# Kernel optimization log

Hardware: AMD Instinct MI355X
Metric: run time of the kernel (lower is better)

Reference implementation:

```python
import jax, jax.numpy as jnp
import numpy as np

B, N, DIM, H = 1, 768, 384, 12
SK, SV, PK, PV, PD = 16, 16, 4, 4, 128
NUM_LOGITS = 3
SCALAR_SCALE = (NUM_LOGITS * SK) ** -0.5
POINT_SCALE = (NUM_LOGITS * PK * (9.0 / 2.0)) ** -0.5
PAIR_SCALE = NUM_LOGITS ** -0.5
EPS = 1e-8
SOFTPLUS_INV_1 = float(np.log(np.e - 1.0))  # torch init: log(exp(1)-1)


def setup_inputs() -> dict:
    key = jax.random.key(0)
    ks = jax.random.split(key, 16)
    w = lambda k, shape: (jax.random.normal(k, shape, jnp.float32) * 0.02)
    return {
        "single_repr": jax.random.normal(ks[0], (B, N, DIM), jnp.float32),
        "pairwise_repr": jax.random.normal(ks[1], (B, N, N, PD), jnp.float32),
        "rotations": jax.random.normal(ks[2], (B, N, 3, 3), jnp.float32),
        "translations": jax.random.normal(ks[3], (B, N, 3), jnp.float32),
        "mask": jnp.ones((B, N), dtype=bool),
        "Wq_s": w(ks[4], (DIM, H * SK)),
        "Wk_s": w(ks[5], (DIM, H * SK)),
        "Wv_s": w(ks[6], (DIM, H * SV)),
        "Wq_p": w(ks[7], (DIM, H * PK * 3)),
        "Wk_p": w(ks[8], (DIM, H * PK * 3)),
        "Wv_p": w(ks[9], (DIM, H * PV * 3)),
        "W_pair": w(ks[10], (PD, H)),
        "b_pair": jnp.zeros((H,), jnp.float32),
        "point_weights": jnp.full((H,), SOFTPLUS_INV_1, jnp.float32),
        "W_out": w(ks[11], (H * (SV + PD + PV * 4), DIM)),
        "b_out": jnp.zeros((DIM,), jnp.float32),
    }


def _ipa(single_repr, pairwise_repr, rotations, translations, mask,
         Wq_s, Wk_s, Wv_s, Wq_p, Wk_p, Wv_p, W_pair, b_pair,
         point_weights, W_out, b_out):
    x = single_repr
    # scalar q/k/v: (b,n,h*d) -> (b,h,n,d)
    heads_s = lambda t, d: t.reshape(B, N, H, d).transpose(0, 2, 1, 3)
    q_s = heads_s(x @ Wq_s, SK)
    k_s = heads_s(x @ Wk_s, SK)
    v_s = heads_s(x @ Wv_s, SV)
    # point q/k/v: (b,n,h*d*3) -> (b,h,n,d,3), then apply global frame
    heads_p = lambda t, d: t.reshape(B, N, H, d, 3).transpose(0, 2, 1, 3, 4)
    trans = translations[:, None, :, None, :]  # (b,1,n,1,3)
    to_global = lambda t: jnp.einsum('bhndc,bnrc->bhndr', t, rotations) + trans
    q_p = to_global(heads_p(x @ Wq_p, PK))
    k_p = to_global(heads_p(x @ Wk_p, PK))
    v_p = to_global(heads_p(x @ Wv_p, PV))

    logits = jnp.einsum('bhid,bhjd->bhij', q_s, k_s) * SCALAR_SCALE
    pair_bias = pairwise_repr @ W_pair + b_pair  # (b,i,j,h)
    logits = logits + pair_bias.transpose(0, 3, 1, 2) * PAIR_SCALE
    diff = q_p[:, :, :, None] - k_p[:, :, None]  # (b,h,i,j,d,3)
    point_dist = jnp.sum(diff * diff, axis=(-2, -1))  # (b,h,i,j)
    pw = jax.nn.softplus(point_weights)[None, :, None, None]
    logits = logits - 0.5 * POINT_SCALE * pw * point_dist

    m2 = (mask[:, :, None] & mask[:, None, :])[:, None]  # (b,1,i,j)
    logits = jnp.where(m2, logits, -jnp.finfo(logits.dtype).max)
    attn = jax.nn.softmax(logits, axis=-1)

    r_scalar = jnp.einsum('bhij,bhjd->bhid', attn, v_s)
    r_pair = jnp.einsum('bhij,bijd->bhid', attn, pairwise_repr)
    r_point = jnp.einsum('bhij,bhjdc->bhidc', attn, v_p) - trans
    # back to local frame: multiply by R^T
    r_point = jnp.einsum('bhndc,bncr->bhndr', r_point, rotations)
    r_pnorm = jnp.sqrt(jnp.sum(r_point * r_point, axis=-1) + EPS)

    flat = lambda t: t.transpose(0, 2, 1, 3).reshape(B, N, -1)
    f_point = r_point.transpose(0, 2, 1, 3, 4).reshape(B, N, -1)
    results = jnp.concatenate(
        [flat(r_scalar), f_point, flat(r_pnorm), flat(r_pair)], axis=-1)
    return results @ W_out + b_out


def reference(single_repr, pairwise_repr, rotations, translations, mask,
              Wq_s, Wk_s, Wv_s, Wq_p, Wk_p, Wv_p, W_pair, b_pair,
              point_weights, W_out, b_out):
    return _ipa(single_repr, pairwise_repr, rotations, translations, mask,
                Wq_s, Wk_s, Wv_s, Wq_p, Wk_p, Wv_p, W_pair, b_pair,
                point_weights, W_out, b_out)
```

## Files before the change

kernel.cpp:

```cpp
#include <hip/hip_runtime.h>
#include <math.h>

#define NRES 768
#define DIMM 384
#define NH   12

#define SCALAR_SCALE 0.14433756729740646f
#define HALF_POINT   0.06804138174397717f
#define PAIR_SCALE   0.5773502691896258f

__global__ __launch_bounds__(256) void k1_proj(
    const float* __restrict__ x, const float* __restrict__ rot, const float* __restrict__ trans,
    const float* __restrict__ Wqs, const float* __restrict__ Wks, const float* __restrict__ Wvs,
    const float* __restrict__ Wqp, const float* __restrict__ Wkp, const float* __restrict__ Wvp,
    float* __restrict__ qs, float* __restrict__ ks, float* __restrict__ vs,
    float* __restrict__ qpg, float* __restrict__ kpg, float* __restrict__ vpg)
{
    __shared__ float xs[4 * 384];
    __shared__ float xp[3][4][144];

    const int tid = threadIdx.x;
    const int n0 = blockIdx.x * 4;

    for (int idx = tid; idx < 384; idx += 256) {
        float4 v = ((const float4*)(x + (size_t)n0 * 384))[idx];
        ((float4*)xs)[idx] = v;
    }
    __syncthreads();

    if (tid < 252) {
        const int g = tid;
        int m, c0, wd;
        if (g < 144) { m = g / 48; c0 = (g - m * 48) * 4; wd = 192; }
        else { int z = g - 144; m = 3 + z / 36; c0 = (z - (m - 3) * 36) * 4; wd = 144; }
        const float* Wm = (m==0)?Wqs : (m==1)?Wks : (m==2)?Wvs : (m==3)?Wqp : (m==4)?Wkp : Wvp;
        const float* wp = Wm + c0;
        float acc[4][4] = {};
        #pragma unroll 2
        for (int k = 0; k < DIMM; ++k) {
            float4 w = *(const float4*)wp; wp += wd;
            #pragma unroll
            for (int r = 0; r < 4; ++r) {
                float xv = xs[r * 384 + k];
                acc[r][0] = fmaf(xv, w.x, acc[r][0]);
                acc[r][1] = fmaf(xv, w.y, acc[r][1]);
                acc[r][2] = fmaf(xv, w.z, acc[r][2]);
                acc[r][3] = fmaf(xv, w.w, acc[r][3]);
            }
        }
        if (m < 3) {
            float* dst = (m==0)?qs : (m==1)?ks : vs;
            #pragma unroll
            for (int r = 0; r < 4; ++r) {
                float4 st = make_float4(acc[r][0], acc[r][1], acc[r][2], acc[r][3]);
                *(float4*)(dst + (size_t)(n0 + r) * 192 + c0) = st;
            }
        } else {
            int mi = m - 3;
            #pragma unroll
            for (int r = 0; r < 4; ++r)
                #pragma unroll
                for (int u = 0; u < 4; ++u) xp[mi][r][c0 + u] = acc[r][u];
        }
    }
    __syncthreads();

    for (int t = tid; t < 576; t += 256) {
        int mi = t / 192; int rm = t - mi * 192; int r = rm / 48; int pt = rm - r * 48; int c0 = pt * 3;
        float p0 = xp[mi][r][c0+0], p1 = xp[mi][r][c0+1], p2 = xp[mi][r][c0+2];
        int n = n0 + r;
        const float* R = rot + n * 9; const float* T = trans + n * 3;
        float g0 = fmaf(R[0], p0, fmaf(R[1], p1, fmaf(R[2], p2, T[0])));
        float g1 = fmaf(R[3], p0, fmaf(R[4], p1, fmaf(R[5], p2, T[1])));
        float g2 = fmaf(R[6], p0, fmaf(R[7], p1, fmaf(R[8], p2, T[2])));
        float* dst = (mi==0)?qpg : (mi==1)?kpg : vpg;
        dst[n*144 + c0+0] = g0; dst[n*144 + c0+1] = g1; dst[n*144 + c0+2] = g2;
    }
}

__global__ __launch_bounds__(256, 3) void k2_attn(
    const float* __restrict__ pairwise, const float* __restrict__ rot, const float* __restrict__ trans,
    const float* __restrict__ Wp, const float* __restrict__ bp, const float* __restrict__ ptw,
    const float* __restrict__ qs, const float* __restrict__ ks, const float* __restrict__ vs,
    const float* __restrict__ qpg, const float* __restrict__ kpg, const float* __restrict__ vpg,
    float* __restrict__ results)
{
    __shared__ float Pt[64 * 129];
    __shared__ float PBp[4 * 64 * 13];
    __shared__ float E[64 * 13];
    __shared__ float Qs[192], Qp[144];
    __shared__ float mL[12], lL[12], aL[12], invL[12], hpL[12], bpL[12];
    __shared__ float rp_l[144];

    const int tid = threadIdx.x;
    const int i = blockIdx.x;
    const size_t ri = (size_t)i * 1920;

    if (tid < 48)                    ((float4*)Qs)[tid]      = ((const float4*)(qs  + (size_t)i * 192))[tid];
    if (tid >= 64 && tid < 100)      ((float4*)Qp)[tid - 64] = ((const float4*)(qpg + (size_t)i * 144))[tid - 64];
    if (tid >= 128 && tid < 140) {
        int h = tid - 128;
        hpL[h] = HALF_POINT * log1pf(__expf(ptw[h]));
        bpL[h] = PAIR_SCALE * bp[h];
        mL[h] = -3.0e38f; lL[h] = 0.f;
    }
    __syncthreads();

    const int j  = tid & 63;
    const int hg = tid >> 6;
    const int hh = tid >> 7, dpr = tid & 127, hb = hh * 6;

    float accp[6] = {0.f,0.f,0.f,0.f,0.f,0.f};
    float accs = 0.f, accq = 0.f;
    const int hs = tid >> 4;
    const int hq = tid / 12;

    for (int tile = 0; tile < 12; ++tile) {
        const int j0 = tile * 64;

        {
            const float4* Pg = (const float4*)(pairwise + ((size_t)i * NRES + j0) * 128);
            #pragma unroll
            for (int q = 0; q < 8; ++q) {
                int idx = tid + 256 * q;
                float4 v = Pg[idx];
                int row = idx >> 5, c4 = (idx & 31) << 2;
                float* dp = &Pt[row * 129 + c4];
                dp[0] = v.x; dp[1] = v.y; dp[2] = v.z; dp[3] = v.w;
            }
        }
        __syncthreads();

        {
            float pbp[12];
            #pragma unroll
            for (int h = 0; h < 12; ++h) pbp[h] = 0.f;
            const int d0 = hg * 32;
            #pragma unroll 4
            for (int d = 0; d < 32; ++d) {
                float p = Pt[j * 129 + d0 + d];
                const float* w = Wp + (d0 + d) * 12;
                #pragma unroll
                for (int h = 0; h < 12; ++h) pbp[h] = fmaf(p, w[h], pbp[h]);
            }
            const int jg = j0 + j;
            const float* kr = ks  + (size_t)jg * 192;
            const float* kp = kpg + (size_t)jg * 144;
            float own[3];
            #pragma unroll
            for (int e = 0; e < 3; ++e) {
                int h = 3 * hg + e;
                const float4* kv = (const float4*)(kr + h * 16);
                float4 a0 = kv[0], a1 = kv[1], a2 = kv[2], a3 = kv[3];
                const float4* qv = (const float4*)(Qs + h * 16);
                float4 q0 = qv[0], q1 = qv[1], q2 = qv[2], q3 = qv[3];
                float s = q0.x*a0.x + q0.y*a0.y + q0.z*a0.z + q0.w*a0.w
                        + q1.x*a1.x + q1.y*a1.y + q1.z*a1.z + q1.w*a1.w
                        + q2.x*a2.x + q2.y*a2.y + q2.z*a2.z + q2.w*a2.w
                        + q3.x*a3.x + q3.y*a3.y + q3.z*a3.z + q3.w*a3.w;
                const float4* pv = (const float4*)(kp + h * 12);
                float4 p0 = pv[0], p1 = pv[1], p2 = pv[2];
                const float4* qpv = (const float4*)(Qp + h * 12);
                float4 u0 = qpv[0], u1 = qpv[1], u2 = qpv[2];
                float d0v, dist;
                d0v = u0.x - p0.x; dist  = d0v*d0v;
                d0v = u0.y - p0.y; dist += d0v*d0v;
                d0v = u0.z - p0.z; dist += d0v*d0v;
                d0v = u0.w - p0.w; dist += d0v*d0v;
                d0v = u1.x - p1.x; dist += d0v*d0v;
                d0v = u1.y - p1.y; dist += d0v*d0v;
                d0v = u1.z - p1.z; dist += d0v*d0v;
                d0v = u1.w - p1.w; dist += d0v*d0v;
                d0v = u2.x - p2.x; dist += d0v*d0v;
                d0v = u2.y - p2.y; dist += d0v*d0v;
                d0v = u2.z - p2.z; dist += d0v*d0v;
                d0v = u2.w - p2.w; dist += d0v*d0v;
                own[e] = SCALAR_SCALE * s - hpL[h] * dist + bpL[h];
            }
            float* pbw = &PBp[hg * 832 + j * 13];
            #pragma unroll
            for (int h = 0; h < 12; ++h) {
                float v = PAIR_SCALE * pbp[h];
                if (h >= 3 * hg && h < 3 * hg + 3) v += own[h - 3 * hg];
                pbw[h] = v;
            }
        }
        __syncthreads();

        {
            const float* pbr = &PBp[j * 13];
            float Lv[3], tm[3];
            #pragma unroll
            for (int e = 0; e < 3; ++e) {
                int h = 3 * hg + e;
                Lv[e] = pbr[h] + pbr[832 + h] + pbr[1664 + h] + pbr[2496 + h];
                tm[e] = Lv[e];
            }
            #pragma unroll
            for (int o = 32; o > 0; o >>= 1) {
                #pragma unroll
                for (int e = 0; e < 3; ++e) tm[e] = fmaxf(tm[e], __shfl_xor(tm[e], o));
            }
            float ss[3], mnv[3], alv[3];
            #pragma unroll
            for (int e = 0; e < 3; ++e) {
                int h = 3 * hg + e;
                float mo = mL[h];
                float mn = fmaxf(mo, tm[e]);
                alv[e] = __expf(mo - mn);
                mnv[e] = mn;
                float ev = __expf(Lv[e] - mn);
                E[j * 13 + h] = ev;
                ss[e] = ev;
            }
            #pragma unroll
            for (int o = 32; o > 0; o >>= 1) {
                #pragma unroll
                for (int e = 0; e < 3; ++e) ss[e] += __shfl_xor(ss[e], o);
            }
            if (j == 0) {
                #pragma unroll
                for (int e = 0; e < 3; ++e) {
                    int h = 3 * hg + e;
                    mL[h] = mnv[e]; aL[h] = alv[e];
                    lL[h] = lL[h] * alv[e] + ss[e];
                }
            }
        }
        __syncthreads();

        {
            #pragma unroll
            for (int u = 0; u < 6; ++u) accp[u] *= aL[hb + u];
            #pragma unroll 4
            for (int jj = 0; jj < 64; ++jj) {
                float p = Pt[jj * 129 + dpr];
                const float* ej = &E[jj * 13 + hb];
                accp[0] = fmaf(ej[0], p, accp[0]);
                accp[1] = fmaf(ej[1], p, accp[1]);
                accp[2] = fmaf(ej[2], p, accp[2]);
                accp[3] = fmaf(ej[3], p, accp[3]);
                accp[4] = fmaf(ej[4], p, accp[4]);
                accp[5] = fmaf(ej[5], p, accp[5]);
            }
        }
        if (tid < 192) {
            accs *= aL[hs];
            const float* vb = vs + (size_t)j0 * 192 + tid;
            #pragma unroll 4
            for (int jj = 0; jj < 64; ++jj)
                accs = fmaf(E[jj * 13 + hs], vb[(size_t)jj * 192], accs);
        }
        if (tid < 144) {
            accq *= aL[hq];
            const float* vb = vpg + (size_t)j0 * 144 + tid;
            #pragma unroll 4
            for (int jj = 0; jj < 64; ++jj)
                accq = fmaf(E[jj * 13 + hq], vb[(size_t)jj * 144], accq);
        }
        __syncthreads();
    }

    if (tid < 12) invL[tid] = 1.0f / lL[tid];
    __syncthreads();

    #pragma unroll
    for (int u = 0; u < 6; ++u)
        results[ri + 384 + (size_t)(hb + u) * 128 + dpr] = accp[u] * invL[hb + u];

    if (tid < 192) results[ri + tid] = accs * invL[hs];

    if (tid < 144) {
        int pc = tid - hq * 12;
        int coord = pc - (pc / 3) * 3;
        rp_l[tid] = accq * invL[hq] - trans[i * 3 + coord];
    }
    __syncthreads();

    if (tid < 48) {
        int h = tid >> 2, d = tid & 3; int c0 = h * 12 + d * 3;
        float p0 = rp_l[c0], p1 = rp_l[c0 + 1], p2 = rp_l[c0 + 2];
        const float* R = rot + i * 9;
        float o0 = p0 * R[0] + p1 * R[3] + p2 * R[6];
        float o1 = p0 * R[1] + p1 * R[4] + p2 * R[7];
        float o2 = p0 * R[2] + p1 * R[5] + p2 * R[8];
        results[ri + 192 + c0 + 0] = o0;
        results[ri + 192 + c0 + 1] = o1;
        results[ri + 192 + c0 + 2] = o2;
        results[ri + 336 + h * 4 + d] = sqrtf(o0*o0 + o1*o1 + o2*o2 + 1e-8f);
    }
}

__global__ __launch_bounds__(384) void k3_out(
    const float* __restrict__ results, const float* __restrict__ Wo, const float* __restrict__ bo,
    float* __restrict__ out)
{
    __shared__ float As[4 * 1924];
    __shared__ float red[3 * 96 * 17];

    const int t = threadIdx.x;
    const int r0 = blockIdx.x * 4;

    #pragma unroll
    for (int q = 0; q < 5; ++q) {
        int idx = t + 384 * q;
        if (idx < 1920) {
            int r = idx / 480, c4 = idx - r * 480;
            float4 v = ((const float4*)(results + (size_t)(r0 + r) * 1920))[c4];
            float* dp = &As[r * 1924 + c4 * 4];
            dp[0] = v.x; dp[1] = v.y; dp[2] = v.z; dp[3] = v.w;
        }
    }
    __syncthreads();

    const int cg = t % 96, kp = t / 96;
    float acc[4][4] = {};
    const float* wp = Wo + (size_t)(kp * 480) * 384 + cg * 4;
    int ka = kp * 480;
    #pragma unroll 2
    for (int k = 0; k < 480; ++k, ++ka) {
        float4 w = *(const float4*)wp; wp += 384;
        #pragma unroll
        for (int r = 0; r < 4; ++r) {
            float a = As[r * 1924 + ka];
            acc[r][0] = fmaf(a, w.x, acc[r][0]);
            acc[r][1] = fmaf(a, w.y, acc[r][1]);
            acc[r][2] = fmaf(a, w.z, acc[r][2]);
            acc[r][3] = fmaf(a, w.w, acc[r][3]);
        }
    }
    if (kp > 0) {
        float* rp = &red[((kp - 1) * 96 + cg) * 17];
        #pragma unroll
        for (int r = 0; r < 4; ++r)
            #pragma unroll
            for (int u = 0; u < 4; ++u) rp[r * 4 + u] = acc[r][u];
    }
    __syncthreads();
    if (kp == 0) {
        float4 b = *(const float4*)(bo + cg * 4);
        #pragma unroll
        for (int r = 0; r < 4; ++r) {
            const float* r1 = &red[(0 * 96 + cg) * 17 + r * 4];
            const float* r2 = &red[(1 * 96 + cg) * 17 + r * 4];
            const float* r3 = &red[(2 * 96 + cg) * 17 + r * 4];
            float4 o;
            o.x = acc[r][0] + r1[0] + r2[0] + r3[0] + b.x;
            o.y = acc[r][1] + r1[1] + r2[1] + r3[1] + b.y;
            o.z = acc[r][2] + r1[2] + r2[2] + r3[2] + b.z;
            o.w = acc[r][3] + r1[3] + r2[3] + r3[3] + b.w;
            *(float4*)(out + (size_t)(r0 + r) * 384 + cg * 4) = o;
        }
    }
}

extern "C" void kernel_launch(void* const* d_in, const int* in_sizes, int n_in,
                              void* d_out, int out_size, void* d_ws, size_t ws_size,
                              hipStream_t stream) {
    const float* x        = (const float*)d_in[0];
    const float* pairwise = (const float*)d_in[1];
    const float* rot      = (const float*)d_in[2];
    const float* trans    = (const float*)d_in[3];
    const float* Wqs   = (const float*)d_in[5];
    const float* Wks   = (const float*)d_in[6];
    const float* Wvs   = (const float*)d_in[7];
    const float* Wqp   = (const float*)d_in[8];
    const float* Wkp   = (const float*)d_in[9];
    const float* Wvp   = (const float*)d_in[10];
    const float* Wp    = (const float*)d_in[11];
    const float* bp    = (const float*)d_in[12];
    const float* ptw   = (const float*)d_in[13];
    const float* Wo    = (const float*)d_in[14];
    const float* bo    = (const float*)d_in[15];
    float* out = (float*)d_out;

    float* ws = (float*)d_ws;
    float* qs      = ws;
    float* ksb     = qs   + 147456;
    float* vsb     = ksb  + 147456;
    float* qpg     = vsb  + 147456;
    float* kpg     = qpg  + 110592;
    float* vpg     = kpg  + 110592;
    float* results = vpg  + 110592;

    hipLaunchKernelGGL(k1_proj, dim3(192), dim3(256), 0, stream,
                       x, rot, trans, Wqs, Wks, Wvs, Wqp, Wkp, Wvp,
                       qs, ksb, vsb, qpg, kpg, vpg);
    hipLaunchKernelGGL(k2_attn, dim3(768), dim3(256), 0, stream,
                       pairwise, rot, trans, Wp, bp, ptw,
                       qs, ksb, vsb, qpg, kpg, vpg, results);
    hipLaunchKernelGGL(k3_out, dim3(192), dim3(384), 0, stream,
                       results, Wo, bo, out);
}
```

Baseline: 878.6 us.

## Split pair-bias into separate kernel and restructure attention, projection, and output GEMM

Adds a kernel that computes the pair bias for every (i,h,j) into a workspace buffer. The attention kernel then drops its LDS staging of the pairwise tile and its syncs, double-buffers the exp weights, and reads pairwise straight from global memory for the weighted sum. The projection kernel now handles 2 rows per block instead of 4, and the output GEMM handles 3 rows per block without the split-K reduction. The cost is reading the 300MB pairwise tensor twice (once for the bias, once for the aggregation), plus a fallback path used when the workspace is too small.

```diff
diff --git a/kernel.cpp b/kernel.cpp
--- a/kernel.cpp
+++ b/kernel.cpp
@@ -9,64 +9,53 @@
 #define HALF_POINT   0.06804138174397717f
 #define PAIR_SCALE   0.5773502691896258f
 
-__global__ __launch_bounds__(256) void k1_proj(
+__global__ __launch_bounds__(256) void k1_proj2(
     const float* __restrict__ x, const float* __restrict__ rot, const float* __restrict__ trans,
     const float* __restrict__ Wqs, const float* __restrict__ Wks, const float* __restrict__ Wvs,
     const float* __restrict__ Wqp, const float* __restrict__ Wkp, const float* __restrict__ Wvp,
     float* __restrict__ qs, float* __restrict__ ks, float* __restrict__ vs,
     float* __restrict__ qpg, float* __restrict__ kpg, float* __restrict__ vpg)
 {
-    __shared__ float xs[4 * 384];
-    __shared__ float xp[3][4][144];
+    __shared__ float xs[2 * 384];
+    __shared__ float xp[3][2][144];
 
     const int tid = threadIdx.x;
-    const int n0 = blockIdx.x * 4;
-
-    for (int idx = tid; idx < 384; idx += 256) {
-        float4 v = ((const float4*)(x + (size_t)n0 * 384))[idx];
-        ((float4*)xs)[idx] = v;
-    }
+    const int n0 = blockIdx.x * 2;
+
+    for (int idx = tid; idx < 192; idx += 256)
+        ((float4*)xs)[idx] = ((const float4*)(x + (size_t)n0 * 384))[idx];
     __syncthreads();
 
     if (tid < 252) {
-        const int g = tid;
         int m, c0, wd;
-        if (g < 144) { m = g / 48; c0 = (g - m * 48) * 4; wd = 192; }
-        else { int z = g - 144; m = 3 + z / 36; c0 = (z - (m - 3) * 36) * 4; wd = 144; }
+        if (tid < 144) { m = tid / 48; c0 = (tid - m * 48) * 4; wd = 192; }
+        else { int z = tid - 144; m = 3 + z / 36; c0 = (z - (m - 3) * 36) * 4; wd = 144; }
         const float* Wm = (m==0)?Wqs : (m==1)?Wks : (m==2)?Wvs : (m==3)?Wqp : (m==4)?Wkp : Wvp;
         const float* wp = Wm + c0;
-        float acc[4][4] = {};
-        #pragma unroll 2
+        float a00=0.f,a01=0.f,a02=0.f,a03=0.f, a10=0.f,a11=0.f,a12=0.f,a13=0.f;
+        #pragma unroll 4
         for (int k = 0; k < DIMM; ++k) {
             float4 w = *(const float4*)wp; wp += wd;
-            #pragma unroll
-            for (int r = 0; r < 4; ++r) {
-                float xv = xs[r * 384 + k];
-                acc[r][0] = fmaf(xv, w.x, acc[r][0]);
-                acc[r][1] = fmaf(xv, w.y, acc[r][1]);
-                acc[r][2] = fmaf(xv, w.z, acc[r][2]);
-                acc[r][3] = fmaf(xv, w.w, acc[r][3]);
-            }
+            float x0 = xs[k], x1 = xs[384 + k];
+            a00 = fmaf(x0, w.x, a00); a01 = fmaf(x0, w.y, a01);
+            a02 = fmaf(x0, w.z, a02); a03 = fmaf(x0, w.w, a03);
+            a10 = fmaf(x1, w.x, a10); a11 = fmaf(x1, w.y, a11);
+            a12 = fmaf(x1, w.z, a12); a13 = fmaf(x1, w.w, a13);
         }
         if (m < 3) {
             float* dst = (m==0)?qs : (m==1)?ks : vs;
-            #pragma unroll
-            for (int r = 0; r < 4; ++r) {
-                float4 st = make_float4(acc[r][0], acc[r][1], acc[r][2], acc[r][3]);
-                *(float4*)(dst + (size_t)(n0 + r) * 192 + c0) = st;
-            }
+            *(float4*)(dst + (size_t)(n0    ) * 192 + c0) = make_float4(a00,a01,a02,a03);
+            *(float4*)(dst + (size_t)(n0 + 1) * 192 + c0) = make_float4(a10,a11,a12,a13);
         } else {
             int mi = m - 3;
-            #pragma unroll
-            for (int r = 0; r < 4; ++r)
-                #pragma unroll
-                for (int u = 0; u < 4; ++u) xp[mi][r][c0 + u] = acc[r][u];
-        }
-    }
-    __syncthreads();
-
-    for (int t = tid; t < 576; t += 256) {
-        int mi = t / 192; int rm = t - mi * 192; int r = rm / 48; int pt = rm - r * 48; int c0 = pt * 3;
+            xp[mi][0][c0+0]=a00; xp[mi][0][c0+1]=a01; xp[mi][0][c0+2]=a02; xp[mi][0][c0+3]=a03;
+            xp[mi][1][c0+0]=a10; xp[mi][1][c0+1]=a11; xp[mi][1][c0+2]=a12; xp[mi][1][c0+3]=a13;
+        }
+    }
+    __syncthreads();
+
+    for (int t = tid; t < 288; t += 256) {
+        int r = t / 144; int rem = t - r * 144; int mi = rem / 48; int pt = rem - mi * 48; int c0 = pt * 3;
         float p0 = xp[mi][r][c0+0], p1 = xp[mi][r][c0+1], p2 = xp[mi][r][c0+2];
         int n = n0 + r;
         const float* R = rot + n * 9; const float* T = trans + n * 3;
@@ -78,7 +67,245 @@
     }
 }
 
-__global__ __launch_bounds__(256, 3) void k2_attn(
+__global__ __launch_bounds__(256) void kb_bias(
+    const float* __restrict__ pairwise, const float* __restrict__ Wp, const float* __restrict__ bp,
+    float* __restrict__ PBt)
+{
+    __shared__ float Pt[64 * 129];
+    const int tid = threadIdx.x;
+    const int i  = blockIdx.x / 12;
+    const int j0 = (blockIdx.x - i * 12) * 64;
+
+    const float4* Pg = (const float4*)(pairwise + ((size_t)i * NRES + j0) * 128);
+    #pragma unroll
+    for (int q = 0; q < 8; ++q) {
+        int idx = tid + 256 * q;
+        float4 v = Pg[idx];
+        int row = idx >> 5, c4 = (idx & 31) << 2;
+        float* dp = &Pt[row * 129 + c4];
+        dp[0] = v.x; dp[1] = v.y; dp[2] = v.z; dp[3] = v.w;
+    }
+    __syncthreads();
+
+    const int j = tid & 63, hg = tid >> 6;
+    float b0 = 0.f, b1 = 0.f, b2 = 0.f;
+    const float* prow = &Pt[j * 129];
+    const float* w = Wp + 3 * hg;
+    #pragma unroll 4
+    for (int d = 0; d < 128; ++d) {
+        float p = prow[d];
+        b0 = fmaf(p, w[0], b0);
+        b1 = fmaf(p, w[1], b1);
+        b2 = fmaf(p, w[2], b2);
+        w += 12;
+    }
+    size_t base = ((size_t)i * 12 + 3 * hg) * NRES + j0 + j;
+    PBt[base           ] = PAIR_SCALE * (b0 + bp[3*hg+0]);
+    PBt[base +     NRES] = PAIR_SCALE * (b1 + bp[3*hg+1]);
+    PBt[base + 2 * NRES] = PAIR_SCALE * (b2 + bp[3*hg+2]);
+}
+
+__global__ __launch_bounds__(256, 4) void k2_attn_nb(
+    const float* __restrict__ pairwise, const float* __restrict__ rot, const float* __restrict__ trans,
+    const float* __restrict__ ptw,
+    const float* __restrict__ qs, const float* __restrict__ ks, const float* __restrict__ vs,
+    const float* __restrict__ qpg, const float* __restrict__ kpg, const float* __restrict__ vpg,
+    const float* __restrict__ PBt,
+    float* __restrict__ results)
+{
+    __shared__ float Et[2][12][68];
+    __shared__ float aLb[2][12];
+    __shared__ float Qs[192], Qp[144];
+    __shared__ float mL[12], lL[12], invL[12], hpL[12];
+    __shared__ float rp_l[144];
+
+    const int tid = threadIdx.x;
+    const int i = blockIdx.x;
+    const size_t ri = (size_t)i * 1920;
+
+    if (tid < 48)                    ((float4*)Qs)[tid]      = ((const float4*)(qs  + (size_t)i * 192))[tid];
+    if (tid >= 64 && tid < 100)      ((float4*)Qp)[tid - 64] = ((const float4*)(qpg + (size_t)i * 144))[tid - 64];
+    if (tid >= 128 && tid < 140) {
+        int h = tid - 128;
+        hpL[h] = HALF_POINT * log1pf(__expf(ptw[h]));
+        mL[h] = -3.0e38f; lL[h] = 0.f;
+    }
+    __syncthreads();
+
+    const int j  = tid & 63;
+    const int hg = tid >> 6;
+    const int hh = tid >> 7, dpr = tid & 127, hb = hh * 6;
+
+    float accp[6] = {0.f,0.f,0.f,0.f,0.f,0.f};
+    float accs = 0.f, accq = 0.f;
+    const int hs = tid >> 4;
+    const int hq = tid / 12;
+
+    for (int tile = 0; tile < 12; ++tile) {
+        const int j0 = tile * 64;
+        const int buf = tile & 1;
+
+        float Lv0, Lv1, Lv2;
+        {
+            const size_t pbb = ((size_t)i * 12 + 3 * hg) * NRES + j0 + j;
+            float pb0 = PBt[pbb], pb1 = PBt[pbb + NRES], pb2 = PBt[pbb + 2*NRES];
+            const int jg = j0 + j;
+            const float* kr = ks  + (size_t)jg * 192;
+            const float* kp = kpg + (size_t)jg * 144;
+            float own[3];
+            #pragma unroll
+            for (int e = 0; e < 3; ++e) {
+                int h = 3 * hg + e;
+                const float4* kv = (const float4*)(kr + h * 16);
+                float4 a0 = kv[0], a1 = kv[1], a2 = kv[2], a3 = kv[3];
+                const float4* qv = (const float4*)(Qs + h * 16);
+                float4 q0 = qv[0], q1 = qv[1], q2 = qv[2], q3 = qv[3];
+                float s = q0.x*a0.x + q0.y*a0.y + q0.z*a0.z + q0.w*a0.w
+                        + q1.x*a1.x + q1.y*a1.y + q1.z*a1.z + q1.w*a1.w
+                        + q2.x*a2.x + q2.y*a2.y + q2.z*a2.z + q2.w*a2.w
+                        + q3.x*a3.x + q3.y*a3.y + q3.z*a3.z + q3.w*a3.w;
+                const float4* pv = (const float4*)(kp + h * 12);
+                float4 p0 = pv[0], p1 = pv[1], p2 = pv[2];
+                const float4* qpv = (const float4*)(Qp + h * 12);
+                float4 u0 = qpv[0], u1 = qpv[1], u2 = qpv[2];
+                float dv, dist;
+                dv = u0.x - p0.x; dist  = dv*dv;
+                dv = u0.y - p0.y; dist += dv*dv;
+                dv = u0.z - p0.z; dist += dv*dv;
+                dv = u0.w - p0.w; dist += dv*dv;
+                dv = u1.x - p1.x; dist += dv*dv;
+                dv = u1.y - p1.y; dist += dv*dv;
+                dv = u1.z - p1.z; dist += dv*dv;
+                dv = u1.w - p1.w; dist += dv*dv;
+                dv = u2.x - p2.x; dist += dv*dv;
+                dv = u2.y - p2.y; dist += dv*dv;
+                dv = u2.z - p2.z; dist += dv*dv;
+                dv = u2.w - p2.w; dist += dv*dv;
+                own[e] = SCALAR_SCALE * s - hpL[h] * dist;
+            }
+            Lv0 = own[0] + pb0; Lv1 = own[1] + pb1; Lv2 = own[2] + pb2;
+        }
+
+        {
+            float tm0 = Lv0, tm1 = Lv1, tm2 = Lv2;
+            #pragma unroll
+            for (int o = 32; o > 0; o >>= 1) {
+                tm0 = fmaxf(tm0, __shfl_xor(tm0, o));
+                tm1 = fmaxf(tm1, __shfl_xor(tm1, o));
+                tm2 = fmaxf(tm2, __shfl_xor(tm2, o));
+            }
+            float ss[3], mnv[3], alv[3];
+            float Lvv[3] = {Lv0, Lv1, Lv2};
+            float tmv[3] = {tm0, tm1, tm2};
+            #pragma unroll
+            for (int e = 0; e < 3; ++e) {
+                int h = 3 * hg + e;
+                float mo = mL[h];
+                float mn = fmaxf(mo, tmv[e]);
+                alv[e] = __expf(mo - mn);
+                mnv[e] = mn;
+                float ev = __expf(Lvv[e] - mn);
+                Et[buf][h][j] = ev;
+                ss[e] = ev;
+            }
+            #pragma unroll
+            for (int o = 32; o > 0; o >>= 1) {
+                ss[0] += __shfl_xor(ss[0], o);
+                ss[1] += __shfl_xor(ss[1], o);
+                ss[2] += __shfl_xor(ss[2], o);
+            }
+            if (j == 0) {
+                #pragma unroll
+                for (int e = 0; e < 3; ++e) {
+                    int h = 3 * hg + e;
+                    mL[h] = mnv[e]; aLb[buf][h] = alv[e];
+                    lL[h] = lL[h] * alv[e] + ss[e];
+                }
+            }
+        }
+        __syncthreads();
+
+        {
+            #pragma unroll
+            for (int u = 0; u < 6; ++u) accp[u] *= aLb[buf][hb + u];
+            const float* Prow = pairwise + ((size_t)i * NRES + j0) * 128 + dpr;
+            #pragma unroll 2
+            for (int g = 0; g < 16; ++g) {
+                float4 e0 = *(const float4*)&Et[buf][hb+0][4*g];
+                float4 e1 = *(const float4*)&Et[buf][hb+1][4*g];
+                float4 e2 = *(const float4*)&Et[buf][hb+2][4*g];
+                float4 e3 = *(const float4*)&Et[buf][hb+3][4*g];
+                float4 e4 = *(const float4*)&Et[buf][hb+4][4*g];
+                float4 e5 = *(const float4*)&Et[buf][hb+5][4*g];
+                float p0 = Prow[(size_t)(4*g+0) * 128];
+                float p1 = Prow[(size_t)(4*g+1) * 128];
+                float p2 = Prow[(size_t)(4*g+2) * 128];
+                float p3 = Prow[(size_t)(4*g+3) * 128];
+                accp[0] = fmaf(e0.x,p0,fmaf(e0.y,p1,fmaf(e0.z,p2,fmaf(e0.w,p3,accp[0]))));
+                accp[1] = fmaf(e1.x,p0,fmaf(e1.y,p1,fmaf(e1.z,p2,fmaf(e1.w,p3,accp[1]))));
+                accp[2] = fmaf(e2.x,p0,fmaf(e2.y,p1,fmaf(e2.z,p2,fmaf(e2.w,p3,accp[2]))));
+                accp[3] = fmaf(e3.x,p0,fmaf(e3.y,p1,fmaf(e3.z,p2,fmaf(e3.w,p3,accp[3]))));
+                accp[4] = fmaf(e4.x,p0,fmaf(e4.y,p1,fmaf(e4.z,p2,fmaf(e4.w,p3,accp[4]))));
+                accp[5] = fmaf(e5.x,p0,fmaf(e5.y,p1,fmaf(e5.z,p2,fmaf(e5.w,p3,accp[5]))));
+            }
+        }
+        if (tid < 192) {
+            accs *= aLb[buf][hs];
+            const float* vb = vs + (size_t)j0 * 192 + tid;
+            #pragma unroll 4
+            for (int g = 0; g < 16; ++g) {
+                float4 ev = *(const float4*)&Et[buf][hs][4*g];
+                accs = fmaf(ev.x, vb[(size_t)(4*g+0) * 192], accs);
+                accs = fmaf(ev.y, vb[(size_t)(4*g+1) * 192], accs);
+                accs = fmaf(ev.z, vb[(size_t)(4*g+2) * 192], accs);
+                accs = fmaf(ev.w, vb[(size_t)(4*g+3) * 192], accs);
+            }
+        }
+        if (tid < 144) {
+            accq *= aLb[buf][hq];
+            const float* vb = vpg + (size_t)j0 * 144 + tid;
+            #pragma unroll 4
+            for (int g = 0; g < 16; ++g) {
+                float4 ev = *(const float4*)&Et[buf][hq][4*g];
+                accq = fmaf(ev.x, vb[(size_t)(4*g+0) * 144], accq);
+                accq = fmaf(ev.y, vb[(size_t)(4*g+1) * 144], accq);
+                accq = fmaf(ev.z, vb[(size_t)(4*g+2) * 144], accq);
+                accq = fmaf(ev.w, vb[(size_t)(4*g+3) * 144], accq);
+            }
+        }
+    }
+
+    if (tid < 12) invL[tid] = 1.0f / lL[tid];
+    __syncthreads();
+
+    #pragma unroll
+    for (int u = 0; u < 6; ++u)
+        results[ri + 384 + (size_t)(hb + u) * 128 + dpr] = accp[u] * invL[hb + u];
+
+    if (tid < 192) results[ri + tid] = accs * invL[hs];
+
+    if (tid < 144) {
+        int pc = tid - hq * 12;
+        int coord = pc - (pc / 3) * 3;
+        rp_l[tid] = accq * invL[hq] - trans[i * 3 + coord];
+    }
+    __syncthreads();
+
+    if (tid < 48) {
+        int h = tid >> 2, d = tid & 3; int c0 = h * 12 + d * 3;
+        float p0 = rp_l[c0], p1 = rp_l[c0 + 1], p2 = rp_l[c0 + 2];
+        const float* R = rot + i * 9;
+        float o0 = p0 * R[0] + p1 * R[3] + p2 * R[6];
+        float o1 = p0 * R[1] + p1 * R[4] + p2 * R[7];
+        float o2 = p0 * R[2] + p1 * R[5] + p2 * R[8];
+        results[ri + 192 + c0 + 0] = o0;
+        results[ri + 192 + c0 + 1] = o1;
+        results[ri + 192 + c0 + 2] = o2;
+        results[ri + 336 + h * 4 + d] = sqrtf(o0*o0 + o1*o1 + o2*o2 + 1e-8f);
+    }
+}
+
+__global__ __launch_bounds__(256, 3) void k2_attn_old(
     const float* __restrict__ pairwise, const float* __restrict__ rot, const float* __restrict__ trans,
     const float* __restrict__ Wp, const float* __restrict__ bp, const float* __restrict__ ptw,
     const float* __restrict__ qs, const float* __restrict__ ks, const float* __restrict__ vs,
@@ -117,7 +344,6 @@
 
     for (int tile = 0; tile < 12; ++tile) {
         const int j0 = tile * 64;
-
         {
             const float4* Pg = (const float4*)(pairwise + ((size_t)i * NRES + j0) * 128);
             #pragma unroll
@@ -130,7 +356,6 @@
             }
         }
         __syncthreads();
-
         {
             float pbp[12];
             #pragma unroll
@@ -186,7 +411,6 @@
             }
         }
         __syncthreads();
-
         {
             const float* pbr = &PBp[j * 13];
             float Lv[3], tm[3];
@@ -228,7 +452,6 @@
             }
         }
         __syncthreads();
-
         {
             #pragma unroll
             for (int u = 0; u < 6; ++u) accp[u] *= aL[hb + u];
@@ -291,67 +514,40 @@
     }
 }
 
-__global__ __launch_bounds__(384) void k3_out(
+__global__ __launch_bounds__(384) void k3_out3(
     const float* __restrict__ results, const float* __restrict__ Wo, const float* __restrict__ bo,
     float* __restrict__ out)
 {
-    __shared__ float As[4 * 1924];
-    __shared__ float red[3 * 96 * 17];
+    __shared__ float As[3 * 1936];
 
     const int t = threadIdx.x;
-    const int r0 = blockIdx.x * 4;
+    const int r0 = blockIdx.x * 3;
 
     #pragma unroll
-    for (int q = 0; q < 5; ++q) {
+    for (int q = 0; q < 4; ++q) {
         int idx = t + 384 * q;
-        if (idx < 1920) {
+        if (idx < 1440) {
             int r = idx / 480, c4 = idx - r * 480;
             float4 v = ((const float4*)(results + (size_t)(r0 + r) * 1920))[c4];
-            float* dp = &As[r * 1924 + c4 * 4];
+            float* dp = &As[r * 1936 + c4 * 4];
             dp[0] = v.x; dp[1] = v.y; dp[2] = v.z; dp[3] = v.w;
         }
     }
     __syncthreads();
 
-    const int cg = t % 96, kp = t / 96;
-    float acc[4][4] = {};
-    const float* wp = Wo + (size_t)(kp * 480) * 384 + cg * 4;
-    int ka = kp * 480;
-    #pragma unroll 2
-    for (int k = 0; k < 480; ++k, ++ka) {
-        float4 w = *(const float4*)wp; wp += 384;
-        #pragma unroll
-        for (int r = 0; r < 4; ++r) {
-            float a = As[r * 1924 + ka];
-            acc[r][0] = fmaf(a, w.x, acc[r][0]);
-            acc[r][1] = fmaf(a, w.y, acc[r][1]);
-            acc[r][2] = fmaf(a, w.z, acc[r][2]);
-            acc[r][3] = fmaf(a, w.w, acc[r][3]);
-        }
-    }
-    if (kp > 0) {
-        float* rp = &red[((kp - 1) * 96 + cg) * 17];
-        #pragma unroll
-        for (int r = 0; r < 4; ++r)
-            #pragma unroll
-            for (int u = 0; u < 4; ++u) rp[r * 4 + u] = acc[r][u];
-    }
-    __syncthreads();
-    if (kp == 0) {
-        float4 b = *(const float4*)(bo + cg * 4);
-        #pragma unroll
-        for (int r = 0; r < 4; ++r) {
-            const float* r1 = &red[(0 * 96 + cg) * 17 + r * 4];
-            const float* r2 = &red[(1 * 96 + cg) * 17 + r * 4];
-            const float* r3 = &red[(2 * 96 + cg) * 17 + r * 4];
-            float4 o;
-            o.x = acc[r][0] + r1[0] + r2[0] + r3[0] + b.x;
-            o.y = acc[r][1] + r1[1] + r2[1] + r3[1] + b.y;
-            o.z = acc[r][2] + r1[2] + r2[2] + r3[2] + b.z;
-            o.w = acc[r][3] + r1[3] + r2[3] + r3[3] + b.w;
-            *(float4*)(out + (size_t)(r0 + r) * 384 + cg * 4) = o;
-        }
-    }
+    float acc0 = 0.f, acc1 = 0.f, acc2 = 0.f;
+    const float* wp = Wo + t;
+    #pragma unroll 4
+    for (int k = 0; k < 1920; ++k) {
+        float w = *wp; wp += 384;
+        acc0 = fmaf(As[k], w, acc0);
+        acc1 = fmaf(As[1936 + k], w, acc1);
+        acc2 = fmaf(As[2 * 1936 + k], w, acc2);
+    }
+    float b = bo[t];
+    out[(size_t)(r0 + 0) * 384 + t] = acc0 + b;
+    out[(size_t)(r0 + 1) * 384 + t] = acc1 + b;
+    out[(size_t)(r0 + 2) * 384 + t] = acc2 + b;
 }
 
 extern "C" void kernel_launch(void* const* d_in, const int* in_sizes, int n_in,
@@ -382,13 +578,26 @@
     float* kpg     = qpg  + 110592;
     float* vpg     = kpg  + 110592;
     float* results = vpg  + 110592;
-
-    hipLaunchKernelGGL(k1_proj, dim3(192), dim3(256), 0, stream,
+    float* PBt     = results + 1474560;
+
+    const size_t need = (size_t)(147456*3 + 110592*3 + 1474560 + 7077888) * 4;
+
+    hipLaunchKernelGGL(k1_proj2, dim3(384), dim3(256), 0, stream,
                        x, rot, trans, Wqs, Wks, Wvs, Wqp, Wkp, Wvp,
                        qs, ksb, vsb, qpg, kpg, vpg);
-    hipLaunchKernelGGL(k2_attn, dim3(768), dim3(256), 0, stream,
-                       pairwise, rot, trans, Wp, bp, ptw,
-                       qs, ksb, vsb, qpg, kpg, vpg, results);
-    hipLaunchKernelGGL(k3_out, dim3(192), dim3(384), 0, stream,
+
+    if (ws_size >= need) {
+        hipLaunchKernelGGL(kb_bias, dim3(9216), dim3(256), 0, stream,
+                           pairwise, Wp, bp, PBt);
+        hipLaunchKernelGGL(k2_attn_nb, dim3(768), dim3(256), 0, stream,
+                           pairwise, rot, trans, ptw,
+                           qs, ksb, vsb, qpg, kpg, vpg, PBt, results);
+    } else {
+        hipLaunchKernelGGL(k2_attn_old, dim3(768), dim3(256), 0, stream,
+                           pairwise, rot, trans, Wp, bp, ptw,
+                           qs, ksb, vsb, qpg, kpg, vpg, results);
+    }
+
+    hipLaunchKernelGGL(k3_out3, dim3(256), dim3(384), 0, stream,
                        results, Wo, bo, out);
 }
```

After: 1.006 ms. +14.4%, slower.
